# Kernel tuning notes

Hardware: AMD Instinct MI355X
Metric: run time of the kernel (lower is better)

The kernel has to match this reference:

```python
import jax, jax.numpy as jnp
import numpy as np

MARGIN = 1.0  # init kwarg margin=1.0 (temperature is unused in the original forward)


def setup_inputs() -> dict:
    key = jax.random.key(0)
    k1, k2, k3 = jax.random.split(key, 3)
    B, N = 64, 1024
    predictions = jax.random.normal(k1, (B, N), dtype=jnp.float32)
    targets = jax.random.normal(k2, (B, N), dtype=jnp.float32)
    nan_mask = jax.random.uniform(k3, (B, N)) < 0.1
    targets = jnp.where(nan_mask, jnp.nan, targets)
    return {"predictions": predictions, "targets": targets}


def reference(predictions, targets):
    B, N = predictions.shape
    dt = predictions.dtype
    valid = ~jnp.isnan(targets)                       # [B, N]
    n_valid = valid.sum(-1)                           # [B]
    sample_ok = n_valid > 1                           # samples with >=2 valid items

    t = jnp.nan_to_num(targets)                       # NaNs never used thanks to pair_mask
    # off-diagonal valid-pair mask (equivalent to compacting valid entries then eye==0)
    pair_mask = (valid[:, :, None] & valid[:, None, :]) & (~jnp.eye(N, dtype=bool))[None]
    pm = pair_mask.astype(dt)                         # [B, N, N]

    pred_diff = predictions[:, :, None] - predictions[:, None, :]   # pred_i - pred_j
    target_order = (t[:, :, None] > t[:, None, :]).astype(dt)
    loss = jax.nn.relu(MARGIN - pred_diff) * target_order \
         + jax.nn.relu(MARGIN + pred_diff) * (1.0 - target_order)

    cnt = (n_valid * (n_valid - 1)).astype(dt)        # == pm.sum over last two dims
    sample_loss = (loss * pm).sum((-2, -1)) / jnp.maximum(cnt, 1.0)  # [B]

    num_ok = sample_ok.sum().astype(dt)
    mean_loss = (sample_loss * sample_ok.astype(dt)).sum() / jnp.maximum(num_ok, 1.0)
    return jnp.where(num_ok > 0, mean_loss, jnp.zeros((), dt))
```

## Files before the change

kernel.cpp:

```cpp
#include <hip/hip_runtime.h>


#define BN 1024
#define NB 64

__global__ __launch_bounds__(256) void prl_pairs(const float* __restrict__ P,
                                                 const float* __restrict__ T,
                                                 float* __restrict__ ws_loss) {
    const int b    = blockIdx.x >> 4;
    const int part = blockIdx.x & 15;
    const int prow = part >> 2;
    const int pj   = part & 3;
    const int tid  = threadIdx.x;

    __shared__ __align__(16) float sp[256];
    __shared__ __align__(16) float st[256];

    const int jbase = pj * 256;
    sp[tid] = P[b * BN + jbase + tid];
    st[tid] = T[b * BN + jbase + tid];
    __syncthreads();

    const int i = prow * 256 + tid;
    const float pi = P[b * BN + i];
    const float ti = T[b * BN + i];
    const bool vi = (ti == ti);

    float acc = 0.0f;
    if (vi) {
        const float4* sp4 = (const float4*)sp;
        const float4* st4 = (const float4*)st;
        #pragma unroll 8
        for (int jj = 0; jj < 64; ++jj) {
            const float4 p4 = sp4[jj];
            const float4 t4 = st4[jj];
            {
                float d = pi - p4.x;
                float l = (ti > t4.x) ? fmaxf(1.0f - d, 0.0f) : fmaxf(1.0f + d, 0.0f);
                acc += (t4.x == t4.x) ? l : 0.0f;
            }
            {
                float d = pi - p4.y;
                float l = (ti > t4.y) ? fmaxf(1.0f - d, 0.0f) : fmaxf(1.0f + d, 0.0f);
                acc += (t4.y == t4.y) ? l : 0.0f;
            }
            {
                float d = pi - p4.z;
                float l = (ti > t4.z) ? fmaxf(1.0f - d, 0.0f) : fmaxf(1.0f + d, 0.0f);
                acc += (t4.z == t4.z) ? l : 0.0f;
            }
            {
                float d = pi - p4.w;
                float l = (ti > t4.w) ? fmaxf(1.0f - d, 0.0f) : fmaxf(1.0f + d, 0.0f);
                acc += (t4.w == t4.w) ? l : 0.0f;
            }
        }
        if (prow == pj) acc -= 1.0f;
    }

    #pragma unroll
    for (int off = 32; off > 0; off >>= 1) acc += __shfl_down(acc, off);
    __shared__ float wsum[4];
    const int wid = tid >> 6, lane = tid & 63;
    if (lane == 0) wsum[wid] = acc;
    __syncthreads();
    if (tid == 0) {
        float s = wsum[0] + wsum[1] + wsum[2] + wsum[3];
        atomicAdd(&ws_loss[b], s);
    }
}

__global__ __launch_bounds__(256) void prl_sample(const float* __restrict__ T,
                                                  const float* __restrict__ ws_loss,
                                                  float* __restrict__ ws_acc) {
    const int b = blockIdx.x;
    const int tid = threadIdx.x;
    int cnt = 0;
    #pragma unroll
    for (int k = tid; k < BN; k += 256) {
        float t = T[b * BN + k];
        cnt += (t == t) ? 1 : 0;
    }
    #pragma unroll
    for (int off = 32; off > 0; off >>= 1) cnt += __shfl_down(cnt, off);
    __shared__ int wcnt[4];
    const int wid = tid >> 6, lane = tid & 63;
    if (lane == 0) wcnt[wid] = cnt;
    __syncthreads();
    if (tid == 0) {
        int nv = wcnt[0] + wcnt[1] + wcnt[2] + wcnt[3];
        float c = (float)nv * (float)(nv - 1);
        float sl = ws_loss[b] / fmaxf(c, 1.0f);
        if (nv > 1) {
            atomicAdd(&ws_acc[0], sl);
            atomicAdd(&ws_acc[1], 1.0f);
        }
    }
}

__global__ void prl_final(const float* __restrict__ ws_acc, float* __restrict__ out) {
    float s = ws_acc[0], n = ws_acc[1];
    out[0] = (n > 0.0f) ? (s / n) : 0.0f;
}

extern "C" void kernel_launch(void* const* d_in, const int* in_sizes, int n_in,
                              void* d_out, int out_size, void* d_ws, size_t ws_size,
                              hipStream_t stream) {
    const float* P = (const float*)d_in[0];
    const float* T = (const float*)d_in[1];
    float* out = (float*)d_out;

    float* ws_loss = (float*)d_ws;
    float* ws_acc  = ws_loss + NB;

    hipMemsetAsync(d_ws, 0, (NB + 2) * sizeof(float), stream);

    prl_pairs <<<NB * 16, 256, 0, stream>>>(P, T, ws_loss);
    prl_sample<<<NB,      256, 0, stream>>>(T, ws_loss, ws_acc);
    prl_final <<<1,       1,   0, stream>>>(ws_acc, out);
}
```

Measured before the change: 77.14 us.

## Mask invalid columns with -inf sentinels and drop memset/atomics via deterministic partials

Each block now covers all 1024 rows against a 64-column slice. Invalid columns are stored as -inf so the hinge loss comes out zero without an explicit NaN mask, and the difference is folded into precomputed 1-p and 1+p terms. The valid counts come from a ballot in the pairs kernel, which removes the separate count kernel. The memset and atomics are replaced by per-block partial sums reduced in one 64-thread final kernel. This cuts the launch count and the per-pair ALU work, at the cost of more register pressure from four accumulators per thread.

After: 64.19 us. -16.8%, faster.

```diff
diff --git a/kernel.cpp b/kernel.cpp
--- a/kernel.cpp
+++ b/kernel.cpp
@@ -1,106 +1,104 @@
 #include <hip/hip_runtime.h>
+#include <math.h>
 
 
 #define BN 1024
 #define NB 64
+#define NPART 16
+#define JP 64
 
 __global__ __launch_bounds__(256) void prl_pairs(const float* __restrict__ P,
                                                  const float* __restrict__ T,
-                                                 float* __restrict__ ws_loss) {
-    const int b    = blockIdx.x >> 4;
-    const int part = blockIdx.x & 15;
-    const int prow = part >> 2;
-    const int pj   = part & 3;
-    const int tid  = threadIdx.x;
+                                                 float* __restrict__ ws_part,
+                                                 int* __restrict__ ws_cnt) {
+    const int blk = blockIdx.x;
+    const int b   = blk >> 4;
+    const int q   = blk & 15;
+    const int tid = threadIdx.x;
 
-    __shared__ __align__(16) float sp[256];
-    __shared__ __align__(16) float st[256];
+    __shared__ __align__(16) float sp[JP];
+    __shared__ __align__(16) float st[JP];
 
-    const int jbase = pj * 256;
-    sp[tid] = P[b * BN + jbase + tid];
-    st[tid] = T[b * BN + jbase + tid];
+    if (tid < JP) {
+        float t = T[b * BN + q * JP + tid];
+        float p = P[b * BN + q * JP + tid];
+        bool v = (t == t);
+        st[tid] = v ? t : -INFINITY;
+        sp[tid] = v ? p : -INFINITY;
+        unsigned long long m = __ballot(v);
+        if (tid == 0) ws_cnt[blk] = __popcll(m);
+    }
     __syncthreads();
 
-    const int i = prow * 256 + tid;
-    const float pi = P[b * BN + i];
-    const float ti = T[b * BN + i];
-    const bool vi = (ti == ti);
+    float pi[4], ti[4], a1[4], b1[4], acc[4];
+    #pragma unroll
+    for (int r = 0; r < 4; ++r) {
+        int i = tid + r * 256;
+        pi[r]  = P[b * BN + i];
+        ti[r]  = T[b * BN + i];
+        a1[r]  = 1.0f - pi[r];
+        b1[r]  = 1.0f + pi[r];
+        acc[r] = 0.0f;
+    }
 
-    float acc = 0.0f;
-    if (vi) {
-        const float4* sp4 = (const float4*)sp;
-        const float4* st4 = (const float4*)st;
-        #pragma unroll 8
-        for (int jj = 0; jj < 64; ++jj) {
-            const float4 p4 = sp4[jj];
-            const float4 t4 = st4[jj];
-            {
-                float d = pi - p4.x;
-                float l = (ti > t4.x) ? fmaxf(1.0f - d, 0.0f) : fmaxf(1.0f + d, 0.0f);
-                acc += (t4.x == t4.x) ? l : 0.0f;
-            }
-            {
-                float d = pi - p4.y;
-                float l = (ti > t4.y) ? fmaxf(1.0f - d, 0.0f) : fmaxf(1.0f + d, 0.0f);
-                acc += (t4.y == t4.y) ? l : 0.0f;
-            }
-            {
-                float d = pi - p4.z;
-                float l = (ti > t4.z) ? fmaxf(1.0f - d, 0.0f) : fmaxf(1.0f + d, 0.0f);
-                acc += (t4.z == t4.z) ? l : 0.0f;
-            }
-            {
-                float d = pi - p4.w;
-                float l = (ti > t4.w) ? fmaxf(1.0f - d, 0.0f) : fmaxf(1.0f + d, 0.0f);
-                acc += (t4.w == t4.w) ? l : 0.0f;
-            }
+    const float4* sp4 = (const float4*)sp;
+    const float4* st4 = (const float4*)st;
+    #pragma unroll
+    for (int jj = 0; jj < JP / 4; ++jj) {
+        const float4 p4 = sp4[jj];
+        const float4 t4 = st4[jj];
+        #pragma unroll
+        for (int r = 0; r < 4; ++r) {
+            float e0 = (ti[r] > t4.x) ? (a1[r] + p4.x) : (b1[r] - p4.x);
+            acc[r] += fmaxf(e0, 0.0f);
+            float e1 = (ti[r] > t4.y) ? (a1[r] + p4.y) : (b1[r] - p4.y);
+            acc[r] += fmaxf(e1, 0.0f);
+            float e2 = (ti[r] > t4.z) ? (a1[r] + p4.z) : (b1[r] - p4.z);
+            acc[r] += fmaxf(e2, 0.0f);
+            float e3 = (ti[r] > t4.w) ? (a1[r] + p4.w) : (b1[r] - p4.w);
+            acc[r] += fmaxf(e3, 0.0f);
         }
-        if (prow == pj) acc -= 1.0f;
+    }
+
+    float total = 0.0f;
+    #pragma unroll
+    for (int r = 0; r < 4; ++r) {
+        int i = tid + r * 256;
+        float v = acc[r] - (((i >> 6) == q) ? 1.0f : 0.0f);
+        bool vi = (ti[r] == ti[r]);
+        total += vi ? v : 0.0f;
     }
 
     #pragma unroll
-    for (int off = 32; off > 0; off >>= 1) acc += __shfl_down(acc, off);
+    for (int off = 32; off > 0; off >>= 1) total += __shfl_down(total, off);
     __shared__ float wsum[4];
     const int wid = tid >> 6, lane = tid & 63;
-    if (lane == 0) wsum[wid] = acc;
+    if (lane == 0) wsum[wid] = total;
     __syncthreads();
-    if (tid == 0) {
-        float s = wsum[0] + wsum[1] + wsum[2] + wsum[3];
-        atomicAdd(&ws_loss[b], s);
-    }
+    if (tid == 0) ws_part[blk] = wsum[0] + wsum[1] + wsum[2] + wsum[3];
 }
 
-__global__ __launch_bounds__(256) void prl_sample(const float* __restrict__ T,
-                                                  const float* __restrict__ ws_loss,
-                                                  float* __restrict__ ws_acc) {
-    const int b = blockIdx.x;
-    const int tid = threadIdx.x;
-    int cnt = 0;
+__global__ __launch_bounds__(64) void prl_final(const float* __restrict__ ws_part,
+                                                const int* __restrict__ ws_cnt,
+                                                float* __restrict__ out) {
+    const int s = threadIdx.x;
+    float S = 0.0f;
+    int   n = 0;
     #pragma unroll
-    for (int k = tid; k < BN; k += 256) {
-        float t = T[b * BN + k];
-        cnt += (t == t) ? 1 : 0;
+    for (int k = 0; k < NPART; ++k) {
+        S += ws_part[s * NPART + k];
+        n += ws_cnt[s * NPART + k];
     }
+    float c  = (float)n * (float)(n - 1);
+    float sl = S / fmaxf(c, 1.0f);
+    float ok = (n > 1) ? 1.0f : 0.0f;
+    float num = sl * ok;
     #pragma unroll
-    for (int off = 32; off > 0; off >>= 1) cnt += __shfl_down(cnt, off);
-    __shared__ int wcnt[4];
-    const int wid = tid >> 6, lane = tid & 63;
-    if (lane == 0) wcnt[wid] = cnt;
-    __syncthreads();
-    if (tid == 0) {
-        int nv = wcnt[0] + wcnt[1] + wcnt[2] + wcnt[3];
-        float c = (float)nv * (float)(nv - 1);
-        float sl = ws_loss[b] / fmaxf(c, 1.0f);
-        if (nv > 1) {
-            atomicAdd(&ws_acc[0], sl);
-            atomicAdd(&ws_acc[1], 1.0f);
-        }
+    for (int off = 32; off > 0; off >>= 1) {
+        num += __shfl_down(num, off);
+        ok  += __shfl_down(ok, off);
     }
-}
-
-__global__ void prl_final(const float* __restrict__ ws_acc, float* __restrict__ out) {
-    float s = ws_acc[0], n = ws_acc[1];
-    out[0] = (n > 0.0f) ? (s / n) : 0.0f;
+    if (s == 0) out[0] = (ok > 0.0f) ? (num / ok) : 0.0f;
 }
 
 extern "C" void kernel_launch(void* const* d_in, const int* in_sizes, int n_in,
@@ -110,12 +108,9 @@
     const float* T = (const float*)d_in[1];
     float* out = (float*)d_out;
 
-    float* ws_loss = (float*)d_ws;
-    float* ws_acc  = ws_loss + NB;
+    float* ws_part = (float*)d_ws;
+    int*   ws_cnt  = (int*)(ws_part + NB * NPART);
 
-    hipMemsetAsync(d_ws, 0, (NB + 2) * sizeof(float), stream);
-
-    prl_pairs <<<NB * 16, 256, 0, stream>>>(P, T, ws_loss);
-    prl_sample<<<NB,      256, 0, stream>>>(T, ws_loss, ws_acc);
-    prl_final <<<1,       1,   0, stream>>>(ws_acc, out);
+    prl_pairs<<<NB * NPART, 256, 0, stream>>>(P, T, ws_part, ws_cnt);
+    prl_final<<<1, 64, 0, stream>>>(ws_part, ws_cnt, out);
 }
```
